# Kernel optimization log

Measured on AMD Instinct MI355X. Metric: run time of the kernel, lower is better.

## Reference

```python
import jax, jax.numpy as jnp
import numpy as np

N = 100000          # total nodes
E = 3200000         # total edges (avg degree 32)
B = 100             # num graphs
NPG = N // B        # nodes per graph (uniform -> to_dense_batch is a reshape)
D_IN, D_H, D_E, N_CLS = 128, 64, 32, 10


def setup_inputs() -> dict:
    key = jax.random.key(0)
    ks = jax.random.split(key, 12)
    x = jax.random.normal(ks[0], (N, D_IN), jnp.float32)
    # edges strictly within each graph: offset by graph block
    epg = E // B
    offs = (jnp.arange(E, dtype=jnp.int32) // epg) * NPG
    src = jax.random.randint(ks[1], (E,), 0, NPG, jnp.int32) + offs
    dst = jax.random.randint(ks[2], (E,), 0, NPG, jnp.int32) + offs
    edge_index = jnp.stack([src, dst])
    batch = jnp.repeat(jnp.arange(B, dtype=jnp.int32), NPG)

    def glorot(k, fi, fo):
        return jax.random.normal(k, (fi, fo), jnp.float32) * (1.0 / np.sqrt(fi))

    return {
        "x": x, "edge_index": edge_index, "batch": batch,
        "W_a1": glorot(ks[3], D_IN, D_H), "b_a1": jnp.zeros((D_H,), jnp.float32),
        "W_a2": glorot(ks[4], D_H, D_E),  "b_a2": jnp.zeros((D_E,), jnp.float32),
        "W_x1": glorot(ks[5], D_IN, D_H), "b_x1": jnp.zeros((D_H,), jnp.float32),
        "W_x2": glorot(ks[6], D_H, D_E),  "b_x2": jnp.zeros((D_E,), jnp.float32),
        "W_lin": glorot(ks[7], D_E * D_E, N_CLS),
        "b_lin": jnp.zeros((N_CLS,), jnp.float32),
    }


def _gcn(x, W, b, src, dst, n):
    """PyG GCNConv(improved=True): sym-norm with self-loop weight 2."""
    h = x @ W                                                   # [n, out]
    deg = jax.ops.segment_sum(jnp.ones_like(dst, h.dtype), dst, n) + 2.0
    dinv = jax.lax.rsqrt(deg)                                   # [n]
    coef = dinv[src] * dinv[dst]                                # [E]
    agg = jax.ops.segment_sum(h[src] * coef[:, None], dst, n)   # gather-scatter
    agg = agg + (2.0 * dinv * dinv)[:, None] * h                # self-loop term
    return agg + b


def _segment_softmax(v, seg, nseg):
    m = jax.ops.segment_max(v, seg, nseg)
    e = jnp.exp(v - m[seg])
    s = jax.ops.segment_sum(e, seg, nseg)
    return e / s[seg]


def reference(x, edge_index, batch, W_a1, b_a1, W_a2, b_a2,
              W_x1, b_x1, W_x2, b_x2, W_lin, b_lin):
    src, dst = edge_index[0], edge_index[1]
    n = x.shape[0]
    a1 = jax.nn.relu(_gcn(x, W_a1, b_a1, src, dst, n))
    a2 = _segment_softmax(_gcn(a1, W_a2, b_a2, src, dst, n), batch, B)
    x1 = jax.nn.relu(_gcn(x, W_x1, b_x1, src, dst, n))
    x2 = jax.nn.relu(_gcn(x1, W_x2, b_x2, src, dst, n))
    # uniform graph sizes -> to_dense_batch is a reshape (no padding needed)
    a_b = a2.reshape(B, NPG, D_E)
    x_b = x2.reshape(B, NPG, D_E)
    prods = jnp.einsum('bne,bnf->bef', a_b, x_b)   # bmm(a^T, x): [B, D_E, D_E]
    flat = prods.reshape(B, D_E * D_E)
    return jax.nn.softmax(flat @ W_lin + b_lin, axis=-1)
```

## Files before the change

### kernel.cpp

```cpp
#include <hip/hip_runtime.h>
#include <hip/hip_bf16.h>
#include <hip/hip_fp16.h>

#define N_NODES 100000
#define N_EDGES 3200000
#define NB      100
#define NPG     1000
#define EPG     32000
#define DIN     128
#define DH      64
#define DE      32
#define NCLS    10
#define CNT_BLOCKS  832
#define SORT_BLOCKS 416


typedef _Float16 h2_t __attribute__((ext_vector_type(2)));
typedef _Float16 h8_t __attribute__((ext_vector_type(8)));
typedef float    f4_t __attribute__((ext_vector_type(4)));

__device__ __forceinline__ float dot2f(unsigned a, unsigned b, float c) {
#if __has_builtin(__builtin_amdgcn_fdot2)
    return __builtin_amdgcn_fdot2(__builtin_bit_cast(h2_t, a),
                                  __builtin_bit_cast(h2_t, b), c, false);
#else
    float d;
    asm("v_dot2_f32_f16 %0, %1, %2, %3" : "=v"(d) : "v"(a), "v"(b), "v"(c));
    return d;
#endif
}

#define DOT8(rA, rB, dv)                                                        \
    acc[0] = dot2f(__builtin_amdgcn_perm(rB.x, rA.x, 0x05040100u), dv, acc[0]); \
    acc[1] = dot2f(__builtin_amdgcn_perm(rB.x, rA.x, 0x07060302u), dv, acc[1]); \
    acc[2] = dot2f(__builtin_amdgcn_perm(rB.y, rA.y, 0x05040100u), dv, acc[2]); \
    acc[3] = dot2f(__builtin_amdgcn_perm(rB.y, rA.y, 0x07060302u), dv, acc[3]); \
    acc[4] = dot2f(__builtin_amdgcn_perm(rB.z, rA.z, 0x05040100u), dv, acc[4]); \
    acc[5] = dot2f(__builtin_amdgcn_perm(rB.z, rA.z, 0x07060302u), dv, acc[5]); \
    acc[6] = dot2f(__builtin_amdgcn_perm(rB.w, rA.w, 0x05040100u), dv, acc[6]); \
    acc[7] = dot2f(__builtin_amdgcn_perm(rB.w, rA.w, 0x07060302u), dv, acc[7]);

#define DOTS8(r, pv) do {                                                 \
    unsigned dA_ = __builtin_amdgcn_perm(pv[1], pv[0], 0x07060302u);      \
    unsigned dB_ = __builtin_amdgcn_perm(pv[3], pv[2], 0x07060302u);      \
    unsigned dC_ = __builtin_amdgcn_perm(pv[5], pv[4], 0x07060302u);      \
    unsigned dD_ = __builtin_amdgcn_perm(pv[7], pv[6], 0x07060302u);      \
    DOT8(r[0], r[1], dA_); DOT8(r[2], r[3], dB_);                         \
    DOT8(r[4], r[5], dC_); DOT8(r[6], r[7], dD_); } while (0)

#define LD8(pv, off) { _Pragma("unroll")                                  \
    for (int j_ = 0; j_ < 8; j_++) pv[j_] = ep[(off) + j_]; }

#define GA8H(r, pv) { _Pragma("unroll")                                   \
    for (int j_ = 0; j_ < 8; j_++) r[j_] = hg4[(pv[j_] & 0xffffu) + cl]; }

#define GA8G(r, pv) { _Pragma("unroll")                                   \
    for (int j_ = 0; j_ < 8; j_++) r[j_] = gg4[((pv[j_] & 0xffffu) >> 1) + cl]; }


__global__ __launch_bounds__(256) void k_cnt(const int* __restrict__ dst,
                                             int* __restrict__ cnt8) {
    __shared__ int cnt[NPG];
    int slice = blockIdx.x >> 3;
    int g = (blockIdx.x & 7) + 8 * (slice % 13);
    int sub = slice / 13;
    if (g >= NB) return;
    int t = threadIdx.x;
    for (int i = t; i < NPG; i += 256) cnt[i] = 0;
    __syncthreads();
    int ebase = g * EPG + sub * 4000, nbase = g * NPG;
    for (int i = t; i < 4000; i += 256)
        atomicAdd(&cnt[dst[ebase + i] - nbase], 1);
    __syncthreads();
    for (int i = t; i < NPG; i += 256)
        cnt8[sub * N_NODES + nbase + i] = cnt[i];
}


__global__ __launch_bounds__(1024) void k_scan(const int* __restrict__ cnt8,
                                               int* __restrict__ rowptr,
                                               float* __restrict__ dinv,
                                               unsigned short* __restrict__ dh16) {
    __shared__ int sm[1024];
    int g = (blockIdx.x & 7) + 8 * (blockIdx.x >> 3);
    if (g >= NB) return;
    int t = threadIdx.x;
    int nbase = g * NPG, ebase = g * EPG;
    int v = 0;
    if (t < NPG) {
        #pragma unroll
        for (int s8 = 0; s8 < 8; s8++) v += cnt8[s8 * N_NODES + nbase + t];
        float dv = rsqrtf((float)v + 2.0f);
        dinv[nbase + t] = dv;
        dh16[nbase + t] = __half_as_ushort(__float2half_rn(dv));
    }
    sm[t] = v;
    __syncthreads();
    for (int off = 1; off < 1024; off <<= 1) {
        int xx = (t >= off) ? sm[t - off] : 0;
        __syncthreads();
        sm[t] += xx;
        __syncthreads();
    }
    if (t < NPG)
        rowptr[nbase + t] = ebase + sm[t] - v;
    if (g == NB - 1 && t == 0) rowptr[N_NODES] = N_EDGES;
}


union SharedSG {
    struct {
        int cur[256];
        unsigned buf[10000];
    } sc;
    struct {
        __align__(16) unsigned short wt[16384];
    } ge;
};

__global__ __launch_bounds__(1024) void k_sg(const int* __restrict__ src,
                                             const int* __restrict__ dst,
                                             const float* __restrict__ x,
                                             const float* __restrict__ Wa,
                                             const float* __restrict__ Wx,
                                             const int* __restrict__ rowptr,
                                             const unsigned short* __restrict__ dh16,
                                             unsigned int* __restrict__ esrc,
                                             unsigned short* __restrict__ h16) {
    __shared__ SharedSG S;
    int t = threadIdx.x;
    if (blockIdx.x < SORT_BLOCKS) {
        int xcd = blockIdx.x & 7, slot = blockIdx.x >> 3;
        int g = xcd + 8 * (slot % 13);
        int q = slot / 13;
        if (g >= NB) return;
        int nbase = g * NPG, ebase = g * EPG;
        int n0 = q * 250;
        int base0 = rowptr[nbase + n0];
        int cap = rowptr[nbase + n0 + 250] - base0;
        if (t < 250)
            S.sc.cur[t] = rowptr[nbase + n0 + t] - base0;
        __syncthreads();
        for (int i = t; i < EPG; i += 1024) {
            int d = dst[ebase + i] - nbase - n0;
            if ((unsigned)d < 250u) {
                int s = src[ebase + i];
                int pos = atomicAdd(&S.sc.cur[d], 1);
                S.sc.buf[pos] = ((unsigned)(s - nbase) * 16) |
                                ((unsigned)dh16[s] << 16);
            }
        }
        __syncthreads();
        for (int i = t; i < cap; i += 1024)
            esrc[base0 + i] = S.sc.buf[i];
    } else {
        int b2 = blockIdx.x - SORT_BLOCKS;
        int xcd = b2 & 7, slot = b2 >> 3;
        int g = xcd + 8 * (slot >> 2);
        int chunk = slot & 3;
        if (g >= NB) return;
        int row0 = g * NPG + chunk * 250;
        {
            int cc = t & 127, kg = t >> 7;
            const float* Wp = (cc < 64) ? &Wa[cc] : &Wx[cc - 64];
            #pragma unroll
            for (int j = 0; j < 4; j++) {
                int k0 = kg * 16 + j * 4;
                union { __half h[4]; uint2 u; } pk;
                #pragma unroll
                for (int m = 0; m < 4; m++)
                    pk.h[m] = __float2half_rn(Wp[(k0 + m) * 64]);
                int byte = cc * 256 + ((2 * k0) ^ ((cc & 7) << 4));
                *(uint2*)((char*)S.ge.wt + byte) = pk.u;
            }
        }
        __syncthreads();
        int w = t >> 6, l = t & 63;
        int lr = l & 15, kq = l >> 4;
        int rowA = row0 + w * 16 + lr;
        int rA = rowA < N_NODES ? rowA : N_NODES - 1;
        const float* xr = &x[(size_t)rA * 128];
        h8_t a[4];
        #pragma unroll
        for (int kc = 0; kc < 4; kc++) {
            float4 lo = *(const float4*)&xr[kc * 32 + kq * 8];
            float4 hi = *(const float4*)&xr[kc * 32 + kq * 8 + 4];
            h8_t av;
            av[0] = (_Float16)lo.x; av[1] = (_Float16)lo.y;
            av[2] = (_Float16)lo.z; av[3] = (_Float16)lo.w;
            av[4] = (_Float16)hi.x; av[5] = (_Float16)hi.y;
            av[6] = (_Float16)hi.z; av[7] = (_Float16)hi.w;
            a[kc] = av;
        }
        f4_t acc[8] = {};
        #pragma unroll
        for (int kc = 0; kc < 4; kc++) {
            #pragma unroll
            for (int n = 0; n < 8; n++) {
                int cc = n * 16 + lr;
                int byte = cc * 256 + (((kc * 32 + kq * 8) * 2) ^ ((cc & 7) << 4));
                h8_t bf = *(h8_t*)((char*)S.ge.wt + byte);
                acc[n] = __builtin_amdgcn_mfma_f32_16x16x32_f16(a[kc], bf, acc[n], 0, 0, 0);
            }
        }
        int rowD = row0 + w * 16 + kq * 4;
        #pragma unroll
        for (int n = 0; n < 8; n++) {
            #pragma unroll
            for (int j = 0; j < 4; j++) {
                int r = rowD + j;
                if (r < N_NODES)
                    h16[(size_t)r * 128 + n * 16 + lr] =
                        __half_as_ushort(__float2half_rn(acc[n][j]));
            }
        }
    }
}


__global__ __launch_bounds__(256) void k_agg128(const unsigned short* __restrict__ h16,
                                                const int* __restrict__ rowptr,
                                                const unsigned int* __restrict__ esrc,
                                                const float* __restrict__ dinv,
                                                const float* __restrict__ ba,
                                                const float* __restrict__ bx,
                                                unsigned short* __restrict__ outB16) {
    int xcd = blockIdx.x & 7, slot = blockIdx.x >> 3;
    int gi = slot / 63, chunk = slot - gi * 63;
    int g = xcd + 8 * gi;
    if (g >= NB) return;
    int grp = threadIdx.x >> 4;
    int cl  = threadIdx.x & 15;
    int nl  = chunk * 16 + grp;
    int valid = nl < NPG;
    int nlc = valid ? nl : NPG - 1;
    int wid = g * NPG + nlc;
    const uint4* hg4 = (const uint4*)(h16 + g * NPG * 128);
    float acc[8] = {};
    union U8 { uint4 u; __half h[8]; };
    int e0 = rowptr[wid];
    int e1 = valid ? rowptr[wid + 1] : e0;
    const unsigned* ep = esrc + e0;
    int nb = (e1 - e0) >> 3;
    {
        unsigned pvA[8], pvB[8];
        uint4 rA[8], rB[8];
        if (nb > 0) {
            LD8(pvA, 0); GA8H(rA, pvA);
            if (nb > 1) LD8(pvB, 8);
            int b = 0;
            while (b + 2 < nb) {
                GA8H(rB, pvB); DOTS8(rA, pvA); LD8(pvA, (b + 2) * 8);
                GA8H(rA, pvA); DOTS8(rB, pvB);
                if (b + 3 < nb) LD8(pvB, (b + 3) * 8);
                b += 2;
            }
            if (b + 2 == nb) { GA8H(rB, pvB); DOTS8(rA, pvA); DOTS8(rB, pvB); }
            else             { DOTS8(rA, pvA); }
        }
    }
    int e = e0 + nb * 8;
    for (; e + 2 <= e1; e += 2) {
        unsigned pv0 = esrc[e], pv1 = esrc[e + 1];
        uint4 r0 = hg4[(pv0 & 0xffffu) + cl];
        uint4 r1 = hg4[(pv1 & 0xffffu) + cl];
        unsigned dA = __builtin_amdgcn_perm(pv1, pv0, 0x07060302u);
        DOT8(r0, r1, dA);
    }
    if (e < e1) {
        unsigned pv = esrc[e];
        uint4 r = hg4[(pv & 0xffffu) + cl];
        unsigned dA = pv >> 16;
        DOT8(r, r, dA);
    }
    float di = dinv[wid];
    float sw = 2.0f * di * di;
    U8 hv; hv.u = hg4[nlc * 16 + cl];
    int cl8 = cl * 8;
    const float* bb = (cl8 < 64) ? &ba[cl8] : &bx[cl8 - 64];
    union { __half2 h[4]; uint4 q; } pk;
    #pragma unroll
    for (int k = 0; k < 4; k++) {
        float ox = fmaxf(di * acc[2 * k]     + sw * __half2float(hv.h[2 * k])     + bb[2 * k],     0.0f);
        float oy = fmaxf(di * acc[2 * k + 1] + sw * __half2float(hv.h[2 * k + 1]) + bb[2 * k + 1], 0.0f);
        pk.h[k] = __floats2half2_rn(ox, oy);
    }
    if (valid)
        *(uint4*)&outB16[(size_t)wid * 128 + cl8] = pk.q;
}


__global__ __launch_bounds__(256) void k_agg64(const unsigned short* __restrict__ g16,
                                               const int* __restrict__ rowptr,
                                               const unsigned int* __restrict__ esrc,
                                               const float* __restrict__ dinv,
                                               const float* __restrict__ ba2,
                                               const float* __restrict__ bx2,
                                               float* __restrict__ s2) {
    int xcd = blockIdx.x & 7, slot = blockIdx.x >> 3;
    int gi = slot >> 5, chunk = slot & 31;
    int g = xcd + 8 * gi;
    if (g >= NB) return;
    int grp = threadIdx.x >> 3;
    int cl  = threadIdx.x & 7;
    int nl  = chunk * 32 + grp;
    int valid = nl < NPG;
    int nlc = valid ? nl : NPG - 1;
    int wid = g * NPG + nlc;
    const uint4* gg4 = (const uint4*)(g16 + g * NPG * 64);
    float acc[8] = {};
    union U8 { uint4 u; __half h[8]; };
    int e0 = rowptr[wid];
    int e1 = valid ? rowptr[wid + 1] : e0;
    const unsigned* ep = esrc + e0;
    int nb = (e1 - e0) >> 3;
    {
        unsigned pvA[8], pvB[8];
        uint4 rA[8], rB[8];
        if (nb > 0) {
            LD8(pvA, 0); GA8G(rA, pvA);
            if (nb > 1) LD8(pvB, 8);
            int b = 0;
            while (b + 2 < nb) {
                GA8G(rB, pvB); DOTS8(rA, pvA); LD8(pvA, (b + 2) * 8);
                GA8G(rA, pvA); DOTS8(rB, pvB);
                if (b + 3 < nb) LD8(pvB, (b + 3) * 8);
                b += 2;
            }
            if (b + 2 == nb) { GA8G(rB, pvB); DOTS8(rA, pvA); DOTS8(rB, pvB); }
            else             { DOTS8(rA, pvA); }
        }
    }
    int e = e0 + nb * 8;
    for (; e + 2 <= e1; e += 2) {
        unsigned pv0 = esrc[e], pv1 = esrc[e + 1];
        uint4 r0 = gg4[((pv0 & 0xffffu) >> 1) + cl];
        uint4 r1 = gg4[((pv1 & 0xffffu) >> 1) + cl];
        unsigned dA = __builtin_amdgcn_perm(pv1, pv0, 0x07060302u);
        DOT8(r0, r1, dA);
    }
    if (e < e1) {
        unsigned pv = esrc[e];
        uint4 r = gg4[((pv & 0xffffu) >> 1) + cl];
        unsigned dA = pv >> 16;
        DOT8(r, r, dA);
    }
    float di = dinv[wid];
    float sw = 2.0f * di * di;
    U8 hv; hv.u = gg4[nlc * 8 + cl];
    int cl8 = cl * 8;
    float o[8];
    #pragma unroll
    for (int k = 0; k < 8; k++)
        o[k] = di * acc[k] + sw * __half2float(hv.h[k]);
    if (cl8 < 32) {
        #pragma unroll
        for (int k = 0; k < 8; k++) o[k] += ba2[cl8 + k];
    } else {
        #pragma unroll
        for (int k = 0; k < 8; k++) o[k] = fmaxf(o[k] + bx2[cl8 - 32 + k], 0.0f);
    }
    if (valid) {
        *(float4*)&s2[(size_t)wid * 64 + cl8]     = make_float4(o[0], o[1], o[2], o[3]);
        *(float4*)&s2[(size_t)wid * 64 + cl8 + 4] = make_float4(o[4], o[5], o[6], o[7]);
    }
}


__global__ __launch_bounds__(256) void k_gemm2(const unsigned short* __restrict__ Bm16,
                                               const float* __restrict__ Wa2,
                                               const float* __restrict__ Wx2,
                                               unsigned short* __restrict__ g16) {
    __shared__ float xs[64][132];
    __shared__ float ws[64][68];
    int xcd = blockIdx.x & 7, slot = blockIdx.x >> 3;
    int g = xcd + 8 * (slot >> 4);
    int chunk = slot & 15;
    if (g >= NB) return;
    int row0 = g * NPG + chunk * 64;
    int t = threadIdx.x;
    for (int i = 0; i < 4; i++) {
        int idx = t + 256 * i;
        int k = idx >> 4, c4 = idx & 15, c = c4 * 4;
        float4 v;
        if (c < 32) v = *(const float4*)&Wa2[k * 32 + c];
        else        v = *(const float4*)&Wx2[k * 32 + (c - 32)];
        *(float4*)&ws[k][c] = v;
    }
    for (int i = 0; i < 4; i++) {
        int idx = t + 256 * i;
        int r = idx >> 4, c8 = idx & 15;
        int rr = row0 + r; if (rr >= N_NODES) rr = N_NODES - 1;
        union { uint4 u; __half2 h[4]; } pk;
        pk.u = *(const uint4*)&Bm16[(size_t)rr * 128 + c8 * 8];
        float2 f0 = __half22float2(pk.h[0]);
        float2 f1 = __half22float2(pk.h[1]);
        float2 f2 = __half22float2(pk.h[2]);
        float2 f3 = __half22float2(pk.h[3]);
        int cb = c8 * 8;
        *(float4*)&xs[r][cb]     = make_float4(f0.x, f0.y, f1.x, f1.y);
        *(float4*)&xs[r][cb + 4] = make_float4(f2.x, f2.y, f3.x, f3.y);
    }
    __syncthreads();
    int cg = t & 15, rg = t >> 4;
    int koff = (cg < 8) ? 0 : 64;
    float acc[4][4] = {};
    for (int k = 0; k < 64; k++) {
        float4 w = *(float4*)&ws[k][cg * 4];
        float xv[4];
        for (int i = 0; i < 4; i++) xv[i] = xs[rg * 4 + i][koff + k];
        for (int i = 0; i < 4; i++) {
            acc[i][0] += xv[i] * w.x; acc[i][1] += xv[i] * w.y;
            acc[i][2] += xv[i] * w.z; acc[i][3] += xv[i] * w.w;
        }
    }
    for (int i = 0; i < 4; i++) {
        int r = row0 + rg * 4 + i;
        if (r < N_NODES) {
            union { ushort4 u; __half2 h[2]; } pk;
            pk.h[0] = __floats2half2_rn(acc[i][0], acc[i][1]);
            pk.h[1] = __floats2half2_rn(acc[i][2], acc[i][3]);
            *(ushort4*)&g16[(size_t)r * 64 + cg * 4] = pk.u;
        }
    }
}


__global__ __launch_bounds__(512) void k_smax(const float* __restrict__ s2,
                                              float* __restrict__ gmax,
                                              float* __restrict__ sinv) {
    __shared__ float red[16][32];
    int g = (blockIdx.x & 7) + 8 * (blockIdx.x >> 3);
    if (g >= NB) return;
    int t = threadIdx.x;
    int c = t & 31, sub = t >> 5;
    size_t base = (size_t)g * NPG;
    float m = -1e30f;
    for (int n = sub; n < NPG; n += 16)
        m = fmaxf(m, s2[(base + n) * 64 + c]);
    red[sub][c] = m; __syncthreads();
    if (sub == 0) {
        for (int j = 1; j < 16; j++) m = fmaxf(m, red[j][c]);
        red[0][c] = m;
        gmax[g * 32 + c] = m;
    }
    __syncthreads();
    m = red[0][c];
    __syncthreads();
    float sum = 0.0f;
    for (int n = sub; n < NPG; n += 16)
        sum += __expf(s2[(base + n) * 64 + c] - m);
    red[sub][c] = sum; __syncthreads();
    if (sub == 0) {
        for (int j = 1; j < 16; j++) sum += red[j][c];
        sinv[g * 32 + c] = 1.0f / sum;
    }
}


__global__ __launch_bounds__(256) void k_pool(const float* __restrict__ s2,
                                              const float* __restrict__ gmax,
                                              float* __restrict__ prods) {
    __shared__ float ta[25][32];
    __shared__ float tx[25][32];
    __shared__ float gm[32];
    int xcd = blockIdx.x & 7, slot = blockIdx.x >> 3;
    int g = xcd + 8 * (slot >> 3);
    int ch = slot & 7;
    if (g >= NB) return;
    int t = threadIdx.x;
    if (t < 32) gm[t] = gmax[g * 32 + t];
    int e  = t >> 3;
    int f4 = t & 7;
    float a0 = 0.f, a1 = 0.f, a2 = 0.f, a3 = 0.f;
    int base = g * NPG + ch * 125;
    for (int n0 = 0; n0 < 125; n0 += 25) {
        __syncthreads();
        for (int i = t; i < 25 * 16; i += 256) {
            int r = i >> 4, c4 = i & 15;
            float4 v = *(const float4*)&s2[(size_t)(base + n0 + r) * 64 + c4 * 4];
            if (c4 < 8) {
                int cb = c4 * 4;
                v.x = __expf(v.x - gm[cb + 0]);
                v.y = __expf(v.y - gm[cb + 1]);
                v.z = __expf(v.z - gm[cb + 2]);
                v.w = __expf(v.w - gm[cb + 3]);
                *(float4*)&ta[r][cb] = v;
            } else {
                *(float4*)&tx[r][(c4 - 8) * 4] = v;
            }
        }
        __syncthreads();
        #pragma unroll 5
        for (int n = 0; n < 25; n++) {
            float a   = ta[n][e];
            float4 xv = *(float4*)&tx[n][f4 * 4];
            a0 += a * xv.x; a1 += a * xv.y; a2 += a * xv.z; a3 += a * xv.w;
        }
    }
    *(float4*)&prods[((size_t)(g * 8 + ch)) * 1024 + e * 32 + f4 * 4] =
        make_float4(a0, a1, a2, a3);
}


__global__ __launch_bounds__(256) void k_head(const float* __restrict__ prods,
                                              const float* __restrict__ sinv,
                                              const float* __restrict__ Wlin,
                                              const float* __restrict__ blin,
                                              float* __restrict__ out) {
    __shared__ float red[4][NCLS];
    int g = (blockIdx.x & 7) + 8 * (blockIdx.x >> 3);
    if (g >= NB) return;
    int t = threadIdx.x;
    float p[NCLS];
    for (int c = 0; c < NCLS; c++) p[c] = 0.0f;
    const float* pg = &prods[(size_t)g * 8 * 1024];
    for (int j = 0; j < 4; j++) {
        int k = t * 4 + j;
        int e = k >> 5;
        float v = 0.0f;
        #pragma unroll
        for (int q = 0; q < 8; q++) v += pg[q * 1024 + k];
        v *= sinv[g * 32 + e];
        const float* wrow = &Wlin[k * NCLS];
        for (int c = 0; c < NCLS; c++) p[c] += v * wrow[c];
    }
    for (int off = 32; off > 0; off >>= 1)
        for (int c = 0; c < NCLS; c++) p[c] += __shfl_down(p[c], off, 64);
    int wave = t >> 6, lane = t & 63;
    if (lane == 0)
        for (int c = 0; c < NCLS; c++) red[wave][c] = p[c];
    __syncthreads();
    if (t == 0) {
        float logits[NCLS]; float mx = -1e30f;
        for (int c = 0; c < NCLS; c++) {
            logits[c] = red[0][c] + red[1][c] + red[2][c] + red[3][c] + blin[c];
            mx = fmaxf(mx, logits[c]);
        }
        float s = 0.0f;
        for (int c = 0; c < NCLS; c++) { logits[c] = expf(logits[c] - mx); s += logits[c]; }
        float inv = 1.0f / s;
        for (int c = 0; c < NCLS; c++) out[g * NCLS + c] = logits[c] * inv;
    }
}


extern "C" void kernel_launch(void* const* d_in, const int* in_sizes, int n_in,
                              void* d_out, int out_size, void* d_ws, size_t ws_size,
                              hipStream_t stream) {
    const float* x    = (const float*)d_in[0];
    const int*   ei   = (const int*)d_in[1];
    const float* Wa1  = (const float*)d_in[3];
    const float* ba1  = (const float*)d_in[4];
    const float* Wa2  = (const float*)d_in[5];
    const float* ba2  = (const float*)d_in[6];
    const float* Wx1  = (const float*)d_in[7];
    const float* bx1  = (const float*)d_in[8];
    const float* Wx2  = (const float*)d_in[9];
    const float* bx2  = (const float*)d_in[10];
    const float* Wlin = (const float*)d_in[11];
    const float* blin = (const float*)d_in[12];
    float* out = (float*)d_out;

    char* w = (char*)d_ws;
    auto alloc = [&](size_t bytes) -> void* {
        void* p = (void*)w;
        w += (bytes + 255) & ~(size_t)255;
        return p;
    };
    int*            rowptr = (int*)alloc((N_NODES + 1) * sizeof(int));
    int*            cnt8   = (int*)alloc((size_t)8 * N_NODES * sizeof(int));
    float*          dinv   = (float*)alloc(N_NODES * sizeof(float));
    unsigned short* dh16   = (unsigned short*)alloc(N_NODES * sizeof(unsigned short));
    unsigned int*   esrc   = (unsigned int*)alloc((size_t)N_EDGES * sizeof(unsigned int));
    float*          gmax   = (float*)alloc(NB * DE * sizeof(float));
    float*          sinv   = (float*)alloc(NB * DE * sizeof(float));
    float*          prods  = (float*)alloc((size_t)NB * 8 * 1024 * sizeof(float));
    unsigned short* h16    = (unsigned short*)alloc((size_t)N_NODES * 128 * sizeof(unsigned short));
    unsigned short* b16    = (unsigned short*)alloc((size_t)N_NODES * 128 * sizeof(unsigned short));
    unsigned short* g16    = (unsigned short*)alloc((size_t)N_NODES * 64 * sizeof(unsigned short));
    float*          s2     = (float*)alloc((size_t)N_NODES * 64 * sizeof(float));

    const int* srcp = ei;
    const int* dstp = ei + N_EDGES;

    k_cnt<<<CNT_BLOCKS, 256, 0, stream>>>(dstp, cnt8);
    k_scan<<<8 * 13, 1024, 0, stream>>>(cnt8, rowptr, dinv, dh16);
    k_sg<<<SORT_BLOCKS + 8 * 13 * 4, 1024, 0, stream>>>(srcp, dstp, x, Wa1, Wx1,
                                                        rowptr, dh16, esrc, h16);
    k_agg128<<<8 * 13 * 63, 256, 0, stream>>>(h16, rowptr, esrc, dinv, ba1, bx1, b16);
    k_gemm2<<<8 * 13 * 16, 256, 0, stream>>>(b16, Wa2, Wx2, g16);
    k_agg64<<<8 * 13 * 32, 256, 0, stream>>>(g16, rowptr, esrc, dinv, ba2, bx2, s2);
    k_smax<<<8 * 13, 512, 0, stream>>>(s2, gmax, sinv);
    k_pool<<<8 * 13 * 8, 256, 0, stream>>>(s2, gmax, prods);
    k_head<<<8 * 13, 256, 0, stream>>>(prods, sinv, Wlin, blin, out);
}
```

Before: 310.6 us.

## Fold softmax stats into agg64/pool, MFMA gemm2, shrink gather batches

Removes the separate k_smax kernel. Per-chunk column maxima are now computed in k_agg64 via shared-memory atomicMax on order-preserving keys, and per-chunk exp-sums in k_pool, with k_head finishing the sum reduction. k_gemm2 is rewritten to use MFMA f16 instructions with a swizzled LDS weight tile instead of an fp32 scalar loop. The gather batches in both aggregation kernels drop from 8 to 4 edges and gain launch bounds of 8 blocks per CU, trading memory-level parallelism for occupancy. The k_pool partial sums add ta values, which appear to already be exp(v-max), so the softmax denominators keep the same semantics.

```diff
diff --git a/kernel.cpp b/kernel.cpp
--- a/kernel.cpp
+++ b/kernel.cpp
@@ -40,22 +40,28 @@
     acc[6] = dot2f(__builtin_amdgcn_perm(rB.w, rA.w, 0x05040100u), dv, acc[6]); \
     acc[7] = dot2f(__builtin_amdgcn_perm(rB.w, rA.w, 0x07060302u), dv, acc[7]);
 
-#define DOTS8(r, pv) do {                                                 \
+#define LD4(pv, off) { _Pragma("unroll")                                  \
+    for (int j_ = 0; j_ < 4; j_++) pv[j_] = ep[(off) + j_]; }
+
+#define GA4H(r, pv) { _Pragma("unroll")                                   \
+    for (int j_ = 0; j_ < 4; j_++) r[j_] = hg4[(pv[j_] & 0xffffu) + cl]; }
+
+#define GA4Q(r, pv) { _Pragma("unroll")                                   \
+    for (int j_ = 0; j_ < 4; j_++) r[j_] = gg4[((pv[j_] & 0xffffu) >> 1) + cl]; }
+
+#define DOTS4(r, pv) do {                                                 \
     unsigned dA_ = __builtin_amdgcn_perm(pv[1], pv[0], 0x07060302u);      \
     unsigned dB_ = __builtin_amdgcn_perm(pv[3], pv[2], 0x07060302u);      \
-    unsigned dC_ = __builtin_amdgcn_perm(pv[5], pv[4], 0x07060302u);      \
-    unsigned dD_ = __builtin_amdgcn_perm(pv[7], pv[6], 0x07060302u);      \
-    DOT8(r[0], r[1], dA_); DOT8(r[2], r[3], dB_);                         \
-    DOT8(r[4], r[5], dC_); DOT8(r[6], r[7], dD_); } while (0)
-
-#define LD8(pv, off) { _Pragma("unroll")                                  \
-    for (int j_ = 0; j_ < 8; j_++) pv[j_] = ep[(off) + j_]; }
-
-#define GA8H(r, pv) { _Pragma("unroll")                                   \
-    for (int j_ = 0; j_ < 8; j_++) r[j_] = hg4[(pv[j_] & 0xffffu) + cl]; }
-
-#define GA8G(r, pv) { _Pragma("unroll")                                   \
-    for (int j_ = 0; j_ < 8; j_++) r[j_] = gg4[((pv[j_] & 0xffffu) >> 1) + cl]; }
+    DOT8(r[0], r[1], dA_); DOT8(r[2], r[3], dB_); } while (0)
+
+__device__ __forceinline__ unsigned fenc(float f) {
+    unsigned u = __float_as_uint(f);
+    return u ^ (unsigned)(((int)u >> 31) | (int)0x80000000);
+}
+__device__ __forceinline__ float fdec(unsigned key) {
+    return (key & 0x80000000u) ? __uint_as_float(key ^ 0x80000000u)
+                               : __uint_as_float(~key);
+}
 
 
 __global__ __launch_bounds__(256) void k_cnt(const int* __restrict__ dst,
@@ -218,13 +224,13 @@
 }
 
 
-__global__ __launch_bounds__(256) void k_agg128(const unsigned short* __restrict__ h16,
-                                                const int* __restrict__ rowptr,
-                                                const unsigned int* __restrict__ esrc,
-                                                const float* __restrict__ dinv,
-                                                const float* __restrict__ ba,
-                                                const float* __restrict__ bx,
-                                                unsigned short* __restrict__ outB16) {
+__global__ __launch_bounds__(256, 8) void k_agg128(const unsigned short* __restrict__ h16,
+                                                   const int* __restrict__ rowptr,
+                                                   const unsigned int* __restrict__ esrc,
+                                                   const float* __restrict__ dinv,
+                                                   const float* __restrict__ ba,
+                                                   const float* __restrict__ bx,
+                                                   unsigned short* __restrict__ outB16) {
     int xcd = blockIdx.x & 7, slot = blockIdx.x >> 3;
     int gi = slot / 63, chunk = slot - gi * 63;
     int g = xcd + 8 * gi;
@@ -235,31 +241,31 @@
     int valid = nl < NPG;
     int nlc = valid ? nl : NPG - 1;
     int wid = g * NPG + nlc;
-    const uint4* hg4 = (const uint4*)(h16 + g * NPG * 128);
+    const uint4* hg4 = (const uint4*)(h16 + (size_t)g * NPG * 128);
     float acc[8] = {};
     union U8 { uint4 u; __half h[8]; };
     int e0 = rowptr[wid];
     int e1 = valid ? rowptr[wid + 1] : e0;
     const unsigned* ep = esrc + e0;
-    int nb = (e1 - e0) >> 3;
+    int nb = (e1 - e0) >> 2;
     {
-        unsigned pvA[8], pvB[8];
-        uint4 rA[8], rB[8];
+        unsigned pvA[4], pvB[4];
+        uint4 rA[4], rB[4];
         if (nb > 0) {
-            LD8(pvA, 0); GA8H(rA, pvA);
-            if (nb > 1) LD8(pvB, 8);
+            LD4(pvA, 0); GA4H(rA, pvA);
+            if (nb > 1) LD4(pvB, 4);
             int b = 0;
             while (b + 2 < nb) {
-                GA8H(rB, pvB); DOTS8(rA, pvA); LD8(pvA, (b + 2) * 8);
-                GA8H(rA, pvA); DOTS8(rB, pvB);
-                if (b + 3 < nb) LD8(pvB, (b + 3) * 8);
+                GA4H(rB, pvB); DOTS4(rA, pvA); LD4(pvA, (b + 2) * 4);
+                GA4H(rA, pvA); DOTS4(rB, pvB);
+                if (b + 3 < nb) LD4(pvB, (b + 3) * 4);
                 b += 2;
             }
-            if (b + 2 == nb) { GA8H(rB, pvB); DOTS8(rA, pvA); DOTS8(rB, pvB); }
-            else             { DOTS8(rA, pvA); }
-        }
-    }
-    int e = e0 + nb * 8;
+            if (b + 2 == nb) { GA4H(rB, pvB); DOTS4(rA, pvA); DOTS4(rB, pvB); }
+            else             { DOTS4(rA, pvA); }
+        }
+    }
+    int e = e0 + nb * 4;
     for (; e + 2 <= e1; e += 2) {
         unsigned pv0 = esrc[e], pv1 = esrc[e + 1];
         uint4 r0 = hg4[(pv0 & 0xffffu) + cl];
@@ -278,60 +284,65 @@
     U8 hv; hv.u = hg4[nlc * 16 + cl];
     int cl8 = cl * 8;
     const float* bb = (cl8 < 64) ? &ba[cl8] : &bx[cl8 - 64];
-    union { __half2 h[4]; uint4 q; } pk;
+    union { __half2 h2[4]; uint4 q; } pk;
     #pragma unroll
     for (int k = 0; k < 4; k++) {
         float ox = fmaxf(di * acc[2 * k]     + sw * __half2float(hv.h[2 * k])     + bb[2 * k],     0.0f);
         float oy = fmaxf(di * acc[2 * k + 1] + sw * __half2float(hv.h[2 * k + 1]) + bb[2 * k + 1], 0.0f);
-        pk.h[k] = __floats2half2_rn(ox, oy);
+        pk.h2[k] = __floats2half2_rn(ox, oy);
     }
     if (valid)
         *(uint4*)&outB16[(size_t)wid * 128 + cl8] = pk.q;
 }
 
 
-__global__ __launch_bounds__(256) void k_agg64(const unsigned short* __restrict__ g16,
-                                               const int* __restrict__ rowptr,
-                                               const unsigned int* __restrict__ esrc,
-                                               const float* __restrict__ dinv,
-                                               const float* __restrict__ ba2,
-                                               const float* __restrict__ bx2,
-                                               float* __restrict__ s2) {
+__global__ __launch_bounds__(256, 8) void k_agg64(const unsigned short* __restrict__ g16,
+                                                  const int* __restrict__ rowptr,
+                                                  const unsigned int* __restrict__ esrc,
+                                                  const float* __restrict__ dinv,
+                                                  const float* __restrict__ ba2,
+                                                  const float* __restrict__ bx2,
+                                                  float* __restrict__ s2,
+                                                  float* __restrict__ pmax) {
+    __shared__ unsigned pm[32];
     int xcd = blockIdx.x & 7, slot = blockIdx.x >> 3;
     int gi = slot >> 5, chunk = slot & 31;
     int g = xcd + 8 * gi;
     if (g >= NB) return;
-    int grp = threadIdx.x >> 3;
-    int cl  = threadIdx.x & 7;
+    int t = threadIdx.x;
+    if (t < 32) pm[t] = 0u;
+    __syncthreads();
+    int grp = t >> 3;
+    int cl  = t & 7;
     int nl  = chunk * 32 + grp;
     int valid = nl < NPG;
     int nlc = valid ? nl : NPG - 1;
     int wid = g * NPG + nlc;
-    const uint4* gg4 = (const uint4*)(g16 + g * NPG * 64);
+    const uint4* gg4 = (const uint4*)(g16 + (size_t)g * NPG * 64);
     float acc[8] = {};
     union U8 { uint4 u; __half h[8]; };
     int e0 = rowptr[wid];
     int e1 = valid ? rowptr[wid + 1] : e0;
     const unsigned* ep = esrc + e0;
-    int nb = (e1 - e0) >> 3;
+    int nb = (e1 - e0) >> 2;
     {
-        unsigned pvA[8], pvB[8];
-        uint4 rA[8], rB[8];
+        unsigned pvA[4], pvB[4];
+        uint4 rA[4], rB[4];
         if (nb > 0) {
-            LD8(pvA, 0); GA8G(rA, pvA);
-            if (nb > 1) LD8(pvB, 8);
+            LD4(pvA, 0); GA4Q(rA, pvA);
+            if (nb > 1) LD4(pvB, 4);
             int b = 0;
             while (b + 2 < nb) {
-                GA8G(rB, pvB); DOTS8(rA, pvA); LD8(pvA, (b + 2) * 8);
-                GA8G(rA, pvA); DOTS8(rB, pvB);
-                if (b + 3 < nb) LD8(pvB, (b + 3) * 8);
+                GA4Q(rB, pvB); DOTS4(rA, pvA); LD4(pvA, (b + 2) * 4);
+                GA4Q(rA, pvA); DOTS4(rB, pvB);
+                if (b + 3 < nb) LD4(pvB, (b + 3) * 4);
                 b += 2;
             }
-            if (b + 2 == nb) { GA8G(rB, pvB); DOTS8(rA, pvA); DOTS8(rB, pvB); }
-            else             { DOTS8(rA, pvA); }
-        }
-    }
-    int e = e0 + nb * 8;
+            if (b + 2 == nb) { GA4Q(rB, pvB); DOTS4(rA, pvA); DOTS4(rB, pvB); }
+            else             { DOTS4(rA, pvA); }
+        }
+    }
+    int e = e0 + nb * 4;
     for (; e + 2 <= e1; e += 2) {
         unsigned pv0 = esrc[e], pv1 = esrc[e + 1];
         uint4 r0 = gg4[((pv0 & 0xffffu) >> 1) + cl];
@@ -364,6 +375,14 @@
         *(float4*)&s2[(size_t)wid * 64 + cl8]     = make_float4(o[0], o[1], o[2], o[3]);
         *(float4*)&s2[(size_t)wid * 64 + cl8 + 4] = make_float4(o[4], o[5], o[6], o[7]);
     }
+    if (valid && cl < 4) {
+        #pragma unroll
+        for (int k = 0; k < 8; k++)
+            atomicMax(&pm[cl8 + k], fenc(o[k]));
+    }
+    __syncthreads();
+    if (t < 32)
+        pmax[((size_t)g * 32 + chunk) * 32 + t] = fdec(pm[t]);
 }
 
 
@@ -371,95 +390,69 @@
                                                const float* __restrict__ Wa2,
                                                const float* __restrict__ Wx2,
                                                unsigned short* __restrict__ g16) {
-    __shared__ float xs[64][132];
-    __shared__ float ws[64][68];
+    __shared__ __align__(16) unsigned short wt2[8192];
     int xcd = blockIdx.x & 7, slot = blockIdx.x >> 3;
     int g = xcd + 8 * (slot >> 4);
     int chunk = slot & 15;
     if (g >= NB) return;
     int row0 = g * NPG + chunk * 64;
     int t = threadIdx.x;
-    for (int i = 0; i < 4; i++) {
-        int idx = t + 256 * i;
-        int k = idx >> 4, c4 = idx & 15, c = c4 * 4;
-        float4 v;
-        if (c < 32) v = *(const float4*)&Wa2[k * 32 + c];
-        else        v = *(const float4*)&Wx2[k * 32 + (c - 32)];
-        *(float4*)&ws[k][c] = v;
-    }
-    for (int i = 0; i < 4; i++) {
-        int idx = t + 256 * i;
-        int r = idx >> 4, c8 = idx & 15;
-        int rr = row0 + r; if (rr >= N_NODES) rr = N_NODES - 1;
-        union { uint4 u; __half2 h[4]; } pk;
-        pk.u = *(const uint4*)&Bm16[(size_t)rr * 128 + c8 * 8];
-        float2 f0 = __half22float2(pk.h[0]);
-        float2 f1 = __half22float2(pk.h[1]);
-        float2 f2 = __half22float2(pk.h[2]);
-        float2 f3 = __half22float2(pk.h[3]);
-        int cb = c8 * 8;
-        *(float4*)&xs[r][cb]     = make_float4(f0.x, f0.y, f1.x, f1.y);
-        *(float4*)&xs[r][cb + 4] = make_float4(f2.x, f2.y, f3.x, f3.y);
-    }
-    __syncthreads();
-    int cg = t & 15, rg = t >> 4;
-    int koff = (cg < 8) ? 0 : 64;
-    float acc[4][4] = {};
-    for (int k = 0; k < 64; k++) {
-        float4 w = *(float4*)&ws[k][cg * 4];
-        float xv[4];
-        for (int i = 0; i < 4; i++) xv[i] = xs[rg * 4 + i][koff + k];
-        for (int i = 0; i < 4; i++) {
-            acc[i][0] += xv[i] * w.x; acc[i][1] += xv[i] * w.y;
-            acc[i][2] += xv[i] * w.z; acc[i][3] += xv[i] * w.w;
-        }
-    }
-    for (int i = 0; i < 4; i++) {
-        int r = row0 + rg * 4 + i;
-        if (r < N_NODES) {
-            union { ushort4 u; __half2 h[2]; } pk;
-            pk.h[0] = __floats2half2_rn(acc[i][0], acc[i][1]);
-            pk.h[1] = __floats2half2_rn(acc[i][2], acc[i][3]);
-            *(ushort4*)&g16[(size_t)r * 64 + cg * 4] = pk.u;
-        }
-    }
-}
-
-
-__global__ __launch_bounds__(512) void k_smax(const float* __restrict__ s2,
-                                              float* __restrict__ gmax,
-                                              float* __restrict__ sinv) {
-    __shared__ float red[16][32];
-    int g = (blockIdx.x & 7) + 8 * (blockIdx.x >> 3);
-    if (g >= NB) return;
-    int t = threadIdx.x;
-    int c = t & 31, sub = t >> 5;
-    size_t base = (size_t)g * NPG;
-    float m = -1e30f;
-    for (int n = sub; n < NPG; n += 16)
-        m = fmaxf(m, s2[(base + n) * 64 + c]);
-    red[sub][c] = m; __syncthreads();
-    if (sub == 0) {
-        for (int j = 1; j < 16; j++) m = fmaxf(m, red[j][c]);
-        red[0][c] = m;
-        gmax[g * 32 + c] = m;
-    }
-    __syncthreads();
-    m = red[0][c];
-    __syncthreads();
-    float sum = 0.0f;
-    for (int n = sub; n < NPG; n += 16)
-        sum += __expf(s2[(base + n) * 64 + c] - m);
-    red[sub][c] = sum; __syncthreads();
-    if (sub == 0) {
-        for (int j = 1; j < 16; j++) sum += red[j][c];
-        sinv[g * 32 + c] = 1.0f / sum;
+    {
+        int cc = t & 63, kg = t >> 6;
+        #pragma unroll
+        for (int j = 0; j < 8; j++) {
+            int k0 = kg * 32 + j * 4;
+            union { __half h[4]; uint2 u; } pk;
+            #pragma unroll
+            for (int m = 0; m < 4; m++) {
+                int k = k0 + m;
+                float v;
+                if (cc < 32) v = (k < 64)  ? Wa2[k * 32 + cc] : 0.0f;
+                else         v = (k >= 64) ? Wx2[(k - 64) * 32 + (cc - 32)] : 0.0f;
+                pk.h[m] = __float2half_rn(v);
+            }
+            int byte = cc * 256 + ((2 * k0) ^ ((cc & 7) << 4));
+            *(uint2*)((char*)wt2 + byte) = pk.u;
+        }
+    }
+    __syncthreads();
+    int w = t >> 6, l = t & 63;
+    int lr = l & 15, kq = l >> 4;
+    int rowA = row0 + w * 16 + lr;
+    int rA = rowA < N_NODES ? rowA : N_NODES - 1;
+    const unsigned short* xr = &Bm16[(size_t)rA * 128];
+    h8_t a[4];
+    #pragma unroll
+    for (int kc = 0; kc < 4; kc++)
+        a[kc] = *(const h8_t*)&xr[kc * 32 + kq * 8];
+    f4_t acc[4] = {};
+    #pragma unroll
+    for (int kc = 0; kc < 4; kc++) {
+        #pragma unroll
+        for (int n = 0; n < 4; n++) {
+            int cc = n * 16 + lr;
+            int byte = cc * 256 + (((kc * 32 + kq * 8) * 2) ^ ((cc & 7) << 4));
+            h8_t bf = *(h8_t*)((char*)wt2 + byte);
+            acc[n] = __builtin_amdgcn_mfma_f32_16x16x32_f16(a[kc], bf, acc[n], 0, 0, 0);
+        }
+    }
+    int rowD = row0 + w * 16 + kq * 4;
+    #pragma unroll
+    for (int n = 0; n < 4; n++) {
+        #pragma unroll
+        for (int j = 0; j < 4; j++) {
+            int r = rowD + j;
+            if (r < N_NODES)
+                g16[(size_t)r * 64 + n * 16 + lr] =
+                    __half_as_ushort(__float2half_rn(acc[n][j]));
+        }
     }
 }
 
 
 __global__ __launch_bounds__(256) void k_pool(const float* __restrict__ s2,
-                                              const float* __restrict__ gmax,
+                                              const float* __restrict__ pmax,
+                                              float* __restrict__ psum,
                                               float* __restrict__ prods) {
     __shared__ float ta[25][32];
     __shared__ float tx[25][32];
@@ -469,10 +462,16 @@
     int ch = slot & 7;
     if (g >= NB) return;
     int t = threadIdx.x;
-    if (t < 32) gm[t] = gmax[g * 32 + t];
+    if (t < 32) {
+        float m = -1e30f;
+        for (int j = 0; j < 32; j++)
+            m = fmaxf(m, pmax[((size_t)g * 32 + j) * 32 + t]);
+        gm[t] = m;
+    }
     int e  = t >> 3;
     int f4 = t & 7;
     float a0 = 0.f, a1 = 0.f, a2 = 0.f, a3 = 0.f;
+    float csum = 0.f;
     int base = g * NPG + ch * 125;
     for (int n0 = 0; n0 < 125; n0 += 25) {
         __syncthreads();
@@ -491,6 +490,10 @@
             }
         }
         __syncthreads();
+        if (t < 32) {
+            #pragma unroll 5
+            for (int r = 0; r < 25; r++) csum += ta[r][t];
+        }
         #pragma unroll 5
         for (int n = 0; n < 25; n++) {
             float a   = ta[n][e];
@@ -498,20 +501,29 @@
             a0 += a * xv.x; a1 += a * xv.y; a2 += a * xv.z; a3 += a * xv.w;
         }
     }
+    if (t < 32)
+        psum[((size_t)g * 8 + ch) * 32 + t] = csum;
     *(float4*)&prods[((size_t)(g * 8 + ch)) * 1024 + e * 32 + f4 * 4] =
         make_float4(a0, a1, a2, a3);
 }
 
 
 __global__ __launch_bounds__(256) void k_head(const float* __restrict__ prods,
-                                              const float* __restrict__ sinv,
+                                              const float* __restrict__ psum,
                                               const float* __restrict__ Wlin,
                                               const float* __restrict__ blin,
                                               float* __restrict__ out) {
     __shared__ float red[4][NCLS];
+    __shared__ float sinvv[32];
     int g = (blockIdx.x & 7) + 8 * (blockIdx.x >> 3);
     if (g >= NB) return;
     int t = threadIdx.x;
+    if (t < 32) {
+        float s = 0.f;
+        for (int q = 0; q < 8; q++) s += psum[((size_t)g * 8 + q) * 32 + t];
+        sinvv[t] = 1.0f / s;
+    }
+    __syncthreads();
     float p[NCLS];
     for (int c = 0; c < NCLS; c++) p[c] = 0.0f;
     const float* pg = &prods[(size_t)g * 8 * 1024];
@@ -521,7 +533,7 @@
         float v = 0.0f;
         #pragma unroll
         for (int q = 0; q < 8; q++) v += pg[q * 1024 + k];
-        v *= sinv[g * 32 + e];
+        v *= sinvv[e];
         const float* wrow = &Wlin[k * NCLS];
         for (int c = 0; c < NCLS; c++) p[c] += v * wrow[c];
     }
@@ -573,8 +585,8 @@
     float*          dinv   = (float*)alloc(N_NODES * sizeof(float));
     unsigned short* dh16   = (unsigned short*)alloc(N_NODES * sizeof(unsigned short));
     unsigned int*   esrc   = (unsigned int*)alloc((size_t)N_EDGES * sizeof(unsigned int));
-    float*          gmax   = (float*)alloc(NB * DE * sizeof(float));
-    float*          sinv   = (float*)alloc(NB * DE * sizeof(float));
+    float*          pmax   = (float*)alloc((size_t)NB * 32 * 32 * sizeof(float));
+    float*          psum   = (float*)alloc((size_t)NB * 8 * 32 * sizeof(float));
     float*          prods  = (float*)alloc((size_t)NB * 8 * 1024 * sizeof(float));
     unsigned short* h16    = (unsigned short*)alloc((size_t)N_NODES * 128 * sizeof(unsigned short));
     unsigned short* b16    = (unsigned short*)alloc((size_t)N_NODES * 128 * sizeof(unsigned short));
@@ -590,8 +602,7 @@
                                                         rowptr, dh16, esrc, h16);
     k_agg128<<<8 * 13 * 63, 256, 0, stream>>>(h16, rowptr, esrc, dinv, ba1, bx1, b16);
     k_gemm2<<<8 * 13 * 16, 256, 0, stream>>>(b16, Wa2, Wx2, g16);
-    k_agg64<<<8 * 13 * 32, 256, 0, stream>>>(g16, rowptr, esrc, dinv, ba2, bx2, s2);
-    k_smax<<<8 * 13, 512, 0, stream>>>(s2, gmax, sinv);
-    k_pool<<<8 * 13 * 8, 256, 0, stream>>>(s2, gmax, prods);
-    k_head<<<8 * 13, 256, 0, stream>>>(prods, sinv, Wlin, blin, out);
-}
+    k_agg64<<<8 * 13 * 32, 256, 0, stream>>>(g16, rowptr, esrc, dinv, ba2, bx2, s2, pmax);
+    k_pool<<<8 * 13 * 8, 256, 0, stream>>>(s2, pmax, psum, prods);
+    k_head<<<8 * 13, 256, 0, stream>>>(prods, psum, Wlin, blin, out);
+}
```

Result: slower. 461.1 us (+48.5%).
